# Performance work log

Hardware: AMD Instinct MI355X
Metric: run time of the kernel (lower is better)

Reference implementation:

```python
import jax, jax.numpy as jnp
import numpy as np

H, Hh, E, V, OUT, B, S, T, PAD = 512, 256, 512, 50000, 512, 64, 128, 128, 0


def setup_inputs() -> dict:
    key = jax.random.key(0)
    ks = iter(jax.random.split(key, 32))

    def p(shape, scale=0.05):
        return jax.random.normal(next(ks), shape, jnp.float32) * scale

    emb_in = p((V, E)).at[PAD].set(0.0)   # padding_idx row is zero
    emb_out = p((V, E)).at[PAD].set(0.0)
    src_tokens = jax.random.randint(next(ks), (B, S), 1, V)  # avoid pad_idx=0
    dst = jax.random.randint(next(ks), (B, T), 1, V)
    return {
        'src_tokens': src_tokens,
        'src_lengths': jnp.full((B,), S, dtype=jnp.int32),  # full lengths -> pack/pad is identity
        'dst': dst,
        'emb_in': emb_in, 'emb_out': emb_out,
        'enc_w_ih0': p((2, 4 * Hh, E)),   # [dir, 4h, in] layer0
        'enc_w_ih1': p((2, 4 * Hh, H)),   # layer1 input is bidir concat (H)
        'enc_w_hh': p((2, 2, 4 * Hh, Hh)),  # [layer, dir, 4h, h]
        'enc_b_ih': p((2, 2, 4 * Hh)),
        'enc_b_hh': p((2, 2, 4 * Hh)),
        'dec_w_ih0': p((4 * H, H + E)), 'dec_w_hh0': p((4 * H, H)),
        'dec_b_ih0': p((4 * H,)), 'dec_b_hh0': p((4 * H,)),
        'dec_w_ih1': p((4 * H, H)), 'dec_w_hh1': p((4 * H, H)),
        'dec_b_ih1': p((4 * H,)), 'dec_b_hh1': p((4 * H,)),
        'attn_w': p((H, 2 * H)),           # output_proj, bias=False
        'pred_w': p((OUT, H)), 'pred_b': p((OUT,)),
    }


def _lstm_cell(x, h, c, w_ih, w_hh, b_ih, b_hh):
    # torch gate order: i, f, g, o
    g = x @ w_ih.T + h @ w_hh.T + b_ih + b_hh
    i, f, gg, o = jnp.split(g, 4, axis=-1)
    c = jax.nn.sigmoid(f) * c + jax.nn.sigmoid(i) * jnp.tanh(gg)
    h = jax.nn.sigmoid(o) * jnp.tanh(c)
    return h, c


def _run_lstm(xs, w_ih, w_hh, b_ih, b_hh, reverse):
    z = jnp.zeros((xs.shape[1], w_hh.shape[1]), xs.dtype)

    def step(carry, x):
        h, c = _lstm_cell(x, carry[0], carry[1], w_ih, w_hh, b_ih, b_hh)
        return (h, c), h

    (h, c), out = jax.lax.scan(step, (z, z), xs, reverse=reverse)
    return out, h, c


def _forward(src_tokens, dst, emb_in, emb_out, enc_w_ih0, enc_w_ih1, enc_w_hh,
             enc_b_ih, enc_b_hh, dec_w_ih0, dec_w_hh0, dec_b_ih0, dec_b_hh0,
             dec_w_ih1, dec_w_hh1, dec_b_ih1, dec_b_hh1, attn_w, pred_w, pred_b):
    src = src_tokens.T          # [S, B]
    dst_t = dst.T               # [T, B]
    bsz = src.shape[1]

    # ---- Encoder: 2-layer bidirectional LSTM (sequences are full length) ----
    x = emb_in[src]             # [S, B, E]
    w_ihs = (enc_w_ih0, enc_w_ih1)
    fin_h, fin_c = [], []
    for l in range(2):
        outs = []
        for d, rev in ((0, False), (1, True)):
            o, h, c = _run_lstm(x, w_ihs[l][d], enc_w_hh[l, d], enc_b_ih[l, d], enc_b_hh[l, d], rev)
            outs.append(o)
            fin_h.append(h)
            fin_c.append(c)
        x = jnp.concatenate(outs, axis=-1)   # [S, B, H]
    enc_out = x
    # combine_bidir: per-layer concat of fwd/bwd final states -> [B, H]
    h_l0 = jnp.concatenate(fin_h[0:2], axis=-1)
    h_l1 = jnp.concatenate(fin_h[2:4], axis=-1)
    c_l0 = jnp.concatenate(fin_c[0:2], axis=-1)
    c_l1 = jnp.concatenate(fin_c[2:4], axis=-1)

    enc_mask = (src == PAD)     # [S, B]
    dst_emb = emb_out[dst_t]    # [T, B, E]

    # ---- Decoder: 2 stacked LSTMCells + dot-product attention, input feeding ----
    def dec_step(carry, emb_t):
        h0, c0, h1, c1, feed = carry
        inp = jnp.concatenate((emb_t, feed), axis=1)          # [B, E+H]
        h0, c0 = _lstm_cell(inp, h0, c0, dec_w_ih0, dec_w_hh0, dec_b_ih0, dec_b_hh0)
        h1, c1 = _lstm_cell(h0, h1, c1, dec_w_ih1, dec_w_hh1, dec_b_ih1, dec_b_hh1)
        scores = jnp.einsum('sbh,bh->sb', enc_out, h1)        # [S, B]
        scores = jnp.where(enc_mask, -jnp.inf, scores)
        attn = jax.nn.softmax(scores, axis=0)
        ctx = jnp.einsum('sb,sbh->bh', attn, enc_out)         # [B, H]
        out = jnp.tanh(jnp.concatenate((ctx, h1), axis=1) @ attn_w.T)
        return (h0, c0, h1, c1, out), out

    feed0 = jnp.zeros((bsz, H), dst_emb.dtype)
    _, outs = jax.lax.scan(dec_step, (h_l0, c_l0, h_l1, c_l1, feed0), dst_emb)  # [T, B, H]

    # pred_proj then transpose(1, 2) -> [B, OUT, T]
    res = jnp.einsum('tbh,oh->bot', outs, pred_w) + pred_b[None, :, None]
    return res


def reference(src_tokens, src_lengths, dst, emb_in, emb_out, enc_w_ih0, enc_w_ih1,
              enc_w_hh, enc_b_ih, enc_b_hh, dec_w_ih0, dec_w_hh0, dec_b_ih0,
              dec_b_hh0, dec_w_ih1, dec_w_hh1, dec_b_ih1, dec_b_hh1, attn_w,
              pred_w, pred_b):
    # src_lengths are all == S so pack_padded/pad_packed is an identity
    del src_lengths
    return _forward(src_tokens, dst, emb_in, emb_out, enc_w_ih0, enc_w_ih1,
                    enc_w_hh, enc_b_ih, enc_b_hh, dec_w_ih0, dec_w_hh0,
                    dec_b_ih0, dec_b_hh0, dec_w_ih1, dec_w_hh1, dec_b_ih1,
                    dec_b_hh1, attn_w, pred_w, pred_b)
```

## Files before the change

### kernel.cpp

```cpp
#include <hip/hip_runtime.h>
#include <hip/hip_bf16.h>

#define SS 128
#define TT 128
#define NBLK 256
#define NBD  128
#define FSTRIDE 16

typedef __attribute__((ext_vector_type(8))) short bf16x8;
typedef __attribute__((ext_vector_type(4))) float f32x4;
typedef unsigned short ushort_t;

__device__ __forceinline__ float sigf(float x) { return 1.f / (1.f + __expf(-x)); }

__device__ __forceinline__ ushort_t f2bf(float f) {
  unsigned b = __builtin_bit_cast(unsigned, f);
  return (ushort_t)((b + 0x7FFFu + ((b >> 16) & 1u)) >> 16);
}
__device__ __forceinline__ float bf2f(ushort_t u) {
  return __builtin_bit_cast(float, (unsigned)u << 16);
}

__device__ __forceinline__ void cstoreh(ushort_t* p, ushort_t v) {
  __hip_atomic_store(p, v, __ATOMIC_RELAXED, __HIP_MEMORY_SCOPE_AGENT);
}

__device__ __forceinline__ int xidx(int k, int b) {
  return (((k >> 5) * 256 + b * 4 + ((k >> 3) & 3)) << 3) + (k & 7);
}

template<int NB>
__device__ __forceinline__ void gbar(unsigned* flags, unsigned gen) {
  __syncthreads();
  int tid = threadIdx.x;
  if (tid == 0) {
    asm volatile("s_waitcnt vmcnt(0)" ::: "memory");
    __hip_atomic_store(&flags[blockIdx.x * FSTRIDE], gen, __ATOMIC_RELAXED,
                       __HIP_MEMORY_SCOPE_AGENT);
  }
  {
    int who = tid & (NB - 1);
    int guard = 0;
    while (__hip_atomic_load(&flags[who * FSTRIDE], __ATOMIC_RELAXED,
                             __HIP_MEMORY_SCOPE_AGENT) < gen &&
           ++guard < (1 << 20))
      __builtin_amdgcn_s_sleep(1);
  }
  __syncthreads();
  asm volatile("" ::: "memory");
}

__global__ void k_embed_bf(const float* __restrict__ emb, const int* __restrict__ toks,
                           ushort_t* __restrict__ out, int seqlen) {
  int s = blockIdx.x >> 6, b = blockIdx.x & 63;
  int tok = toks[b * seqlen + s];
  float4 v = ((const float4*)(emb + (size_t)tok * 512))[threadIdx.x];
  unsigned lo = (unsigned)f2bf(v.x) | ((unsigned)f2bf(v.y) << 16);
  unsigned hi = (unsigned)f2bf(v.z) | ((unsigned)f2bf(v.w) << 16);
  uint2 pk = {lo, hi};
  *(uint2*)&out[(size_t)blockIdx.x * 512 + threadIdx.x * 4] = pk;
}

__global__ void k_castw(const float* __restrict__ s0, const float* __restrict__ s1,
                        const float* __restrict__ s2, const float* __restrict__ s3,
                        ushort_t* __restrict__ wBF, ushort_t* __restrict__ predBF) {
  int row = blockIdx.x, which = blockIdx.y;
  if (which == 3 && row >= 512) return;
  const float* src = (which == 0) ? s0 + (size_t)row * 512
                   : (which == 1) ? s1 + (size_t)row * 512
                   : (which == 2) ? s2 + (size_t)row * 1024
                                  : s3 + (size_t)row * 512;
  float4 v = ((const float4*)src)[threadIdx.x];
  unsigned lo = (unsigned)f2bf(v.x) | ((unsigned)f2bf(v.y) << 16);
  unsigned hi = (unsigned)f2bf(v.z) | ((unsigned)f2bf(v.w) << 16);
  uint2 pk = {lo, hi};
  if (which == 3)
    *(uint2*)&predBF[(size_t)row * 512 + threadIdx.x * 4] = pk;
  else
    *(uint2*)&wBF[((size_t)which * 2048 + row) * 512 + threadIdx.x * 4] = pk;
}

__global__ __launch_bounds__(256) void gemm_bf(
    const ushort_t* __restrict__ X, const ushort_t* __restrict__ W,
    const float* __restrict__ b1, const float* __restrict__ b2,
    float* __restrict__ C, int MODE) {
  __shared__ ushort_t Xs[128 * 72];
  __shared__ ushort_t Ws[128 * 72];
  __shared__ float sbias[128];
  int n0 = blockIdx.x * 128, m0 = blockIdx.y * 128;
  int tid = threadIdx.x;
  int lane = tid & 63;
  int wv = __builtin_amdgcn_readfirstlane(tid >> 6);
  int h_m = (wv >> 1) * 64, h_n = (wv & 1) * 64;
  int l16 = lane & 15, l4 = (lane >> 4) * 4, k8 = (lane >> 4) * 8;
  if (tid < 128) sbias[tid] = b1[n0 + tid] + (b2 ? b2[n0 + tid] : 0.f);
  f32x4 acc[4][4] = {};
  int lrow = tid >> 1, lhf = (tid & 1) * 32;
  for (int k0 = 0; k0 < 512; k0 += 64) {
    __syncthreads();
    const ushort_t* xs = X + (size_t)(m0 + lrow) * 512 + k0 + lhf;
    const ushort_t* wsrc = W + (size_t)(n0 + lrow) * 512 + k0 + lhf;
#pragma unroll
    for (int q = 0; q < 4; ++q) {
      *(bf16x8*)&Xs[lrow * 72 + lhf + q * 8] = *(const bf16x8*)(xs + q * 8);
      *(bf16x8*)&Ws[lrow * 72 + lhf + q * 8] = *(const bf16x8*)(wsrc + q * 8);
    }
    __syncthreads();
#pragma unroll
    for (int kk = 0; kk < 2; ++kk) {
#pragma unroll
      for (int mt = 0; mt < 4; ++mt) {
        bf16x8 af = *(const bf16x8*)&Xs[(h_m + mt * 16 + l16) * 72 + kk * 32 + k8];
#pragma unroll
        for (int nt = 0; nt < 4; ++nt) {
          bf16x8 bf = *(const bf16x8*)&Ws[(h_n + nt * 16 + l16) * 72 + kk * 32 + k8];
          acc[mt][nt] = __builtin_amdgcn_mfma_f32_16x16x32_bf16(af, bf, acc[mt][nt], 0, 0, 0);
        }
      }
    }
  }
  if (MODE == 1) {
    int s = (m0 + h_m) >> 6;
#pragma unroll
    for (int nt = 0; nt < 4; ++nt) {
      int n = n0 + h_n + nt * 16 + l16;
      float bias = sbias[h_n + nt * 16 + l16];
#pragma unroll
      for (int mt = 0; mt < 4; ++mt) {
        f32x4 v = acc[mt][nt];
        v[0] += bias; v[1] += bias; v[2] += bias; v[3] += bias;
        *(f32x4*)&C[((size_t)s * 2048 + n) * 64 + mt * 16 + l4] = v;
      }
    }
  } else {
#pragma unroll
    for (int nt = 0; nt < 4; ++nt) {
      int n = n0 + h_n + nt * 16 + l16;
      float bias = sbias[h_n + nt * 16 + l16];
#pragma unroll
      for (int mt = 0; mt < 4; ++mt) {
#pragma unroll
        for (int r = 0; r < 4; ++r) {
          int m = m0 + h_m + mt * 16 + l4 + r;
          C[((size_t)(m & 63) * 512 + n) * 128 + (m >> 6)] = acc[mt][nt][r] + bias;
        }
      }
    }
  }
}

template<int LOUT>
__global__ __launch_bounds__(256, 1) void enc_persist(
    const float* __restrict__ GT,
    const float* __restrict__ whh,
    ushort_t* __restrict__ ringE,
    ushort_t* __restrict__ lout,
    ushort_t* __restrict__ hFin,
    float* __restrict__ cFin,
    unsigned* bar) {
  int nb = blockIdx.x;
  int d = nb >> 7, nbL = nb & 127;
  int tid = threadIdx.x;
  int lane = tid & 63;
  int wv = __builtin_amdgcn_readfirstlane(tid >> 6);
  int l16 = lane & 15, kg = lane >> 4;
  __shared__ ushort_t wE[16 * 264];

  for (int idx = tid; idx < 16 * 256; idx += 256) {
    int m = idx >> 8, k = idx & 255;
    float v = 0.f;
    if (m < 8)
      v = whh[(size_t)d * 262144 +
              (size_t)((m & 3) * 256 + nbL + 128 * (m >> 2)) * 256 + k];
    wE[m * 264 + k] = f2bf(v);
  }
  __syncthreads();

  int b = wv * 16 + l16;
  int hu = nbL + 128 * kg;
  float creg = 0.f;
  const ushort_t* wp = wE + l16 * 264 + kg * 8;

  for (int t = 0; t < SS; ++t) {
    int s = d ? (SS - 1 - t) : t;
    const ushort_t* xb = ringE + (size_t)(t * 2 + d) * 16384 +
                         wv * 512 + l16 * 32 + kg * 8;
    bf16x8 bfr[8];
#pragma unroll
    for (int ks = 0; ks < 8; ++ks) bfr[ks] = *(const bf16x8*)(xb + ks * 2048);
    float gi[4];
    if (lane < 32) {
#pragma unroll
      for (int r = 0; r < 4; ++r)
        gi[r] = GT[((size_t)s * 2048 + d * 1024 + r * 256 + hu) * 64 + b];
    }
    f32x4 acc = {0.f, 0.f, 0.f, 0.f};
#pragma unroll
    for (int ks = 0; ks < 8; ++ks) {
      bf16x8 af = *(const bf16x8*)(wp + ks * 32);
      acc = __builtin_amdgcn_mfma_f32_16x16x32_bf16(af, bfr[ks], acc, 0, 0, 0);
    }
    if (lane < 32) {
      float g4[4];
#pragma unroll
      for (int r = 0; r < 4; ++r) g4[r] = acc[r] + gi[r];
      float ig = sigf(g4[0]), fg = sigf(g4[1]), gg = tanhf(g4[2]), og = sigf(g4[3]);
      creg = fg * creg + ig * gg;
      float hn = og * tanhf(creg);
      cstoreh(&ringE[(size_t)((t + 1) * 2 + d) * 16384 + xidx(hu, b)], f2bf(hn));
      if (LOUT == 0)
        lout[((size_t)s * 64 + b) * 512 + d * 256 + hu] = f2bf(hn);
      else
        lout[(size_t)b * 65536 + (size_t)s * 512 + d * 256 + hu] = f2bf(hn);
      if (t == SS - 1) {
        hFin[xidx(512 + d * 256 + hu, b)] = f2bf(hn);
        cFin[(d * 256 + hu) * 64 + b] = creg;
      }
    }
    if (t < SS - 1) gbar<NBLK>(bar, (unsigned)(t + 1));
  }
}

__global__ __launch_bounds__(256, 1) void dec_persist(
    const float* __restrict__ GdT,
    const float* __restrict__ w_ih0, const float* __restrict__ w_hh0,
    const float* __restrict__ w_ih1, const float* __restrict__ w_hh1,
    const float* __restrict__ b_ih1, const float* __restrict__ b_hh1,
    const float* __restrict__ attn_w,
    const ushort_t* __restrict__ enc_out,
    const int* __restrict__ src_tokens,
    const float* __restrict__ c0T, const float* __restrict__ c1T,
    ushort_t* __restrict__ r0, ushort_t* __restrict__ r1,
    ushort_t* __restrict__ r2,
    ushort_t* __restrict__ houtsB,
    unsigned* bar) {
  int nb = blockIdx.x;
  int tid = threadIdx.x;
  int lane = tid & 63;
  int wv = __builtin_amdgcn_readfirstlane(tid >> 6);
  int l16 = lane & 15, kg = lane >> 4;
  __shared__ ushort_t wAl[16 * 1032];
  __shared__ ushort_t wBl[16 * 1032];
  __shared__ ushort_t wDl[16 * 1032];
  __shared__ float h1s[512];
  __shared__ float sc[128];

  for (int idx = tid; idx < 16384; idx += 256) {
    int m = idx >> 10, k = idx & 1023;
    int j = m >> 2, g = m & 3;
    int row = g * 512 + nb + 128 * j;
    float va = (k < 512) ? w_ih0[(size_t)row * 1024 + 512 + k]
                         : w_hh0[(size_t)row * 512 + (k - 512)];
    float vb = (k < 512) ? w_ih1[(size_t)row * 512 + k]
                         : w_hh1[(size_t)row * 512 + (k - 512)];
    float vd = (m < 4) ? attn_w[(size_t)(nb * 4 + m) * 1024 + k] : 0.f;
    wAl[m * 1032 + k] = f2bf(va);
    wBl[m * 1032 + k] = f2bf(vb);
    wDl[m * 1032 + k] = f2bf(vd);
  }
  __syncthreads();

  int b = wv * 16 + l16;
  int hu = nb + 128 * kg;
  float c0r = c0T[hu * 64 + b];
  float c1r = c1T[hu * 64 + b];
  float bias1[4];
#pragma unroll
  for (int r = 0; r < 4; ++r)
    bias1[r] = b_ih1[r * 512 + hu] + b_hh1[r * 512 + hu];
  const ushort_t* wpA = wAl + l16 * 1032 + kg * 8;
  const ushort_t* wpB = wBl + l16 * 1032 + kg * 8;
  const ushort_t* wpD = wDl + l16 * 1032 + kg * 8;
  int fragoff = wv * 512 + l16 * 32 + kg * 8;

  for (int t = 0; t < TT; ++t) {
    unsigned gb = (unsigned)(t * 4);
    size_t sC = (size_t)t * 65536, sN = (size_t)(t + 1) * 65536;
    {
      const ushort_t* xb = r0 + sC + fragoff;
      bf16x8 bfr[32];
#pragma unroll
      for (int ks = 0; ks < 32; ++ks) bfr[ks] = *(const bf16x8*)(xb + ks * 2048);
      float giA[4];
#pragma unroll
      for (int r = 0; r < 4; ++r)
        giA[r] = GdT[((size_t)t * 2048 + r * 512 + hu) * 64 + b];
      f32x4 acc = {0.f, 0.f, 0.f, 0.f};
#pragma unroll
      for (int ks = 0; ks < 32; ++ks) {
        bf16x8 af = *(const bf16x8*)(wpA + ks * 32);
        acc = __builtin_amdgcn_mfma_f32_16x16x32_bf16(af, bfr[ks], acc, 0, 0, 0);
      }
      float g4[4];
#pragma unroll
      for (int r = 0; r < 4; ++r) g4[r] = acc[r] + giA[r];
      float ig = sigf(g4[0]), fg = sigf(g4[1]), gg = tanhf(g4[2]), og = sigf(g4[3]);
      c0r = fg * c0r + ig * gg;
      float hn = og * tanhf(c0r);
      cstoreh(&r0[sN + xidx(512 + hu, b)], f2bf(hn));
    }
    gbar<NBD>(bar, gb + 1);
    {
      bf16x8 bfr[32];
      const ushort_t* xh0 = r0 + sN + fragoff;
      const ushort_t* xh1 = r1 + sC + fragoff;
#pragma unroll
      for (int ks = 0; ks < 16; ++ks) bfr[ks] = *(const bf16x8*)(xh0 + (16 + ks) * 2048);
#pragma unroll
      for (int ks = 16; ks < 32; ++ks) bfr[ks] = *(const bf16x8*)(xh1 + ks * 2048);
      f32x4 acc = {0.f, 0.f, 0.f, 0.f};
#pragma unroll
      for (int ks = 0; ks < 32; ++ks) {
        bf16x8 af = *(const bf16x8*)(wpB + ks * 32);
        acc = __builtin_amdgcn_mfma_f32_16x16x32_bf16(af, bfr[ks], acc, 0, 0, 0);
      }
      float g4[4];
#pragma unroll
      for (int r = 0; r < 4; ++r) g4[r] = acc[r] + bias1[r];
      float ig = sigf(g4[0]), fg = sigf(g4[1]), gg = tanhf(g4[2]), og = sigf(g4[3]);
      c1r = fg * c1r + ig * gg;
      float hn = og * tanhf(c1r);
      cstoreh(&r1[sN + xidx(512 + hu, b)], f2bf(hn));
    }
    gbar<NBD>(bar, gb + 2);
    if (nb < 64) {
      const ushort_t* eb = enc_out + (size_t)nb * 65536;
      for (int i = tid; i < 512; i += 256)
        h1s[i] = bf2f(r1[sN + xidx(512 + i, nb)]);
      __syncthreads();
      {
        int s2 = tid >> 1, half = tid & 1;
        const ushort_t* er = eb + (size_t)s2 * 512 + half * 256;
        const float* hh = h1s + half * 256;
        float a = 0.f;
#pragma unroll 4
        for (int k = 0; k < 256; k += 8) {
          bf16x8 ev = *(const bf16x8*)(er + k);
#pragma unroll
          for (int i = 0; i < 8; ++i)
            a += bf2f((ushort_t)ev[i]) * hh[k + i];
        }
        a += __shfl_xor(a, 1);
        if (!half) sc[s2] = (src_tokens[nb * SS + s2] == 0) ? -1e30f : a;
      }
      __syncthreads();
      if (tid < 64) {
        float m = fmaxf(sc[tid], sc[tid + 64]);
        for (int off = 32; off; off >>= 1) m = fmaxf(m, __shfl_xor(m, off));
        float e0 = __expf(sc[tid] - m), e1 = __expf(sc[tid + 64] - m);
        float ssum = e0 + e1;
        for (int off = 32; off; off >>= 1) ssum += __shfl_xor(ssum, off);
        float inv = 1.f / ssum;
        sc[tid] = e0 * inv; sc[tid + 64] = e1 * inv;
      }
      __syncthreads();
      float a0 = 0.f, a1 = 0.f;
      for (int s2 = 0; s2 < 128; ++s2) {
        float p_ = sc[s2];
        const ushort_t* er = eb + (size_t)s2 * 512;
        a0 += p_ * bf2f(er[tid]);
        a1 += p_ * bf2f(er[tid + 256]);
      }
      cstoreh(&r2[sC + xidx(tid, nb)], f2bf(a0));
      cstoreh(&r2[sC + xidx(tid + 256, nb)], f2bf(a1));
    }
    gbar<NBD>(bar, gb + 3);
    {
      bf16x8 bfr[32];
      const ushort_t* xc = r2 + sC + fragoff;
      const ushort_t* xh1 = r1 + sN + fragoff;
#pragma unroll
      for (int ks = 0; ks < 16; ++ks) bfr[ks] = *(const bf16x8*)(xc + ks * 2048);
#pragma unroll
      for (int ks = 16; ks < 32; ++ks) bfr[ks] = *(const bf16x8*)(xh1 + ks * 2048);
      f32x4 acc = {0.f, 0.f, 0.f, 0.f};
#pragma unroll
      for (int ks = 0; ks < 32; ++ks) {
        bf16x8 af = *(const bf16x8*)(wpD + ks * 32);
        acc = __builtin_amdgcn_mfma_f32_16x16x32_bf16(af, bfr[ks], acc, 0, 0, 0);
      }
      if (lane < 16) {
#pragma unroll
        for (int r = 0; r < 4; ++r) {
          int o = nb * 4 + r;
          float v = tanhf(acc[r]);
          ushort_t vb = f2bf(v);
          cstoreh(&r0[sN + xidx(o, b)], vb);
          houtsB[((size_t)t * 64 + b) * 512 + o] = vb;
        }
      }
    }
    if (t < TT - 1) gbar<NBD>(bar, gb + 4);
  }
}

extern "C" void kernel_launch(void* const* d_in, const int* in_sizes, int n_in,
                              void* d_out, int out_size, void* d_ws, size_t ws_size,
                              hipStream_t stream) {
  const int*   src_tokens = (const int*)d_in[0];
  const int*   dst        = (const int*)d_in[2];
  const float* emb_in     = (const float*)d_in[3];
  const float* emb_out    = (const float*)d_in[4];
  const float* enc_w_ih0  = (const float*)d_in[5];
  const float* enc_w_ih1  = (const float*)d_in[6];
  const float* enc_w_hh   = (const float*)d_in[7];
  const float* enc_b_ih   = (const float*)d_in[8];
  const float* enc_b_hh   = (const float*)d_in[9];
  const float* dec_w_ih0  = (const float*)d_in[10];
  const float* dec_w_hh0  = (const float*)d_in[11];
  const float* dec_b_ih0  = (const float*)d_in[12];
  const float* dec_b_hh0  = (const float*)d_in[13];
  const float* dec_w_ih1  = (const float*)d_in[14];
  const float* dec_w_hh1  = (const float*)d_in[15];
  const float* dec_b_ih1  = (const float*)d_in[16];
  const float* dec_b_hh1  = (const float*)d_in[17];
  const float* attn_w     = (const float*)d_in[18];
  const float* pred_w     = (const float*)d_in[19];
  const float* pred_b     = (const float*)d_in[20];
  float* out = (float*)d_out;

  float* ws       = (float*)d_ws;
  ushort_t* houtsB = (ushort_t*)ws;
  float* GT       = ws + 4194304;
  ushort_t* encOutB = (ushort_t*)(ws + 20971520);
  ushort_t* predBF  = (ushort_t*)(ws + 23068672);
  ushort_t* r0    = (ushort_t*)(ws + 25165824);
  ushort_t* r1    = (ushort_t*)(ws + 29392896);
  ushort_t* r2    = (ushort_t*)(ws + 33619968);
  ushort_t* wBF   = r2;
  ushort_t* ringE = (ushort_t*)(ws + 37814272);
  float* c0T      = ws + 39927808;
  float* c1T      = ws + 39960576;
  unsigned* barA  = (unsigned*)(ws + 39993344);
  unsigned* barB  = barA + 8192;
  unsigned* barC  = barB + 8192;
  ushort_t* U     = (ushort_t*)(ws + 40017920);

  hipMemsetAsync(barA, 0, 3 * 8192 * sizeof(unsigned), stream);
  hipMemsetAsync(r0, 0, 65536 * sizeof(ushort_t), stream);
  hipMemsetAsync(r1, 0, 65536 * sizeof(ushort_t), stream);
  hipMemsetAsync(ringE, 0, 32768 * sizeof(ushort_t), stream);

  k_castw<<<dim3(2048, 4), 128, 0, stream>>>(enc_w_ih0, enc_w_ih1, dec_w_ih0,
                                             pred_w, wBF, predBF);

  k_embed_bf<<<dim3(8192), 128, 0, stream>>>(emb_in, src_tokens, U, SS);
  gemm_bf<<<dim3(16, 64), 256, 0, stream>>>(U, wBF, enc_b_ih, enc_b_hh, GT, 1);
  enc_persist<0><<<dim3(NBLK), 256, 0, stream>>>(GT, enc_w_hh, ringE, U,
                                                 r0, c0T, barA);
  gemm_bf<<<dim3(16, 64), 256, 0, stream>>>(U, wBF + 1048576,
                                            enc_b_ih + 2048, enc_b_hh + 2048, GT, 1);
  enc_persist<1><<<dim3(NBLK), 256, 0, stream>>>(GT, enc_w_hh + 524288, ringE,
                                                 encOutB, r1, c1T, barB);

  k_embed_bf<<<dim3(8192), 128, 0, stream>>>(emb_out, dst, U, TT);
  gemm_bf<<<dim3(16, 64), 256, 0, stream>>>(U, wBF + 2097152,
                                            dec_b_ih0, dec_b_hh0, GT, 1);

  dec_persist<<<dim3(NBD), 256, 0, stream>>>(
      GT, dec_w_ih0, dec_w_hh0, dec_w_ih1, dec_w_hh1, dec_b_ih1, dec_b_hh1,
      attn_w, encOutB, src_tokens, c0T, c1T, r0, r1, r2, houtsB, barC);

  gemm_bf<<<dim3(4, 64), 256, 0, stream>>>(houtsB, predBF,
                                           pred_b, nullptr, out, 2);
}
```

Before: 4.367 ms.

## Compute attention output projection per batch row locally, removing one grid barrier per step

The decoder's attention output projection (tanh of [ctx,h1] times attn_w) no longer goes through a global ring buffer followed by a grid barrier and an MFMA matvec split across blocks. Each block now keeps its context vector in shared memory and computes all 512 outputs for its own batch row with scalar FMAs over a pre-transposed, packed bf16 copy of attn_w that k_castw builds. This removes one grid-wide barrier and a global round trip per timestep. In exchange each block reads the whole 1 MB weight from global/L2 every step and does the multiply-adds without MFMA.

```diff
diff --git a/kernel.cpp b/kernel.cpp
--- a/kernel.cpp
+++ b/kernel.cpp
@@ -63,9 +63,20 @@
 
 __global__ void k_castw(const float* __restrict__ s0, const float* __restrict__ s1,
                         const float* __restrict__ s2, const float* __restrict__ s3,
-                        ushort_t* __restrict__ wBF, ushort_t* __restrict__ predBF) {
+                        const float* __restrict__ s4,
+                        ushort_t* __restrict__ wBF, ushort_t* __restrict__ predBF,
+                        ushort_t* __restrict__ wTpk) {
   int row = blockIdx.x, which = blockIdx.y;
-  if (which == 3 && row >= 512) return;
+  if (which >= 3 && row >= 512) return;
+  if (which == 4) {
+    int o = row, k0 = threadIdx.x * 8;
+    ushort_t tmp[8];
+#pragma unroll
+    for (int i = 0; i < 8; ++i)
+      tmp[i] = f2bf(s4[(size_t)o * 1024 + k0 + i]);
+    *(bf16x8*)&wTpk[((size_t)threadIdx.x * 512 + o) * 8] = *(const bf16x8*)tmp;
+    return;
+  }
   const float* src = (which == 0) ? s0 + (size_t)row * 512
                    : (which == 1) ? s1 + (size_t)row * 512
                    : (which == 2) ? s2 + (size_t)row * 1024
@@ -226,12 +237,11 @@
     const float* __restrict__ w_ih0, const float* __restrict__ w_hh0,
     const float* __restrict__ w_ih1, const float* __restrict__ w_hh1,
     const float* __restrict__ b_ih1, const float* __restrict__ b_hh1,
-    const float* __restrict__ attn_w,
+    const ushort_t* __restrict__ wTpk,
     const ushort_t* __restrict__ enc_out,
     const int* __restrict__ src_tokens,
     const float* __restrict__ c0T, const float* __restrict__ c1T,
     ushort_t* __restrict__ r0, ushort_t* __restrict__ r1,
-    ushort_t* __restrict__ r2,
     ushort_t* __restrict__ houtsB,
     unsigned* bar) {
   int nb = blockIdx.x;
@@ -241,8 +251,8 @@
   int l16 = lane & 15, kg = lane >> 4;
   __shared__ ushort_t wAl[16 * 1032];
   __shared__ ushort_t wBl[16 * 1032];
-  __shared__ ushort_t wDl[16 * 1032];
   __shared__ float h1s[512];
+  __shared__ float ctxs[512];
   __shared__ float sc[128];
 
   for (int idx = tid; idx < 16384; idx += 256) {
@@ -253,10 +263,8 @@
                          : w_hh0[(size_t)row * 512 + (k - 512)];
     float vb = (k < 512) ? w_ih1[(size_t)row * 512 + k]
                          : w_hh1[(size_t)row * 512 + (k - 512)];
-    float vd = (m < 4) ? attn_w[(size_t)(nb * 4 + m) * 1024 + k] : 0.f;
     wAl[m * 1032 + k] = f2bf(va);
     wBl[m * 1032 + k] = f2bf(vb);
-    wDl[m * 1032 + k] = f2bf(vd);
   }
   __syncthreads();
 
@@ -270,11 +278,10 @@
     bias1[r] = b_ih1[r * 512 + hu] + b_hh1[r * 512 + hu];
   const ushort_t* wpA = wAl + l16 * 1032 + kg * 8;
   const ushort_t* wpB = wBl + l16 * 1032 + kg * 8;
-  const ushort_t* wpD = wDl + l16 * 1032 + kg * 8;
   int fragoff = wv * 512 + l16 * 32 + kg * 8;
 
   for (int t = 0; t < TT; ++t) {
-    unsigned gb = (unsigned)(t * 4);
+    unsigned gb = (unsigned)(t * 3);
     size_t sC = (size_t)t * 65536, sN = (size_t)(t + 1) * 65536;
     {
       const ushort_t* xb = r0 + sC + fragoff;
@@ -354,43 +361,42 @@
         sc[tid] = e0 * inv; sc[tid + 64] = e1 * inv;
       }
       __syncthreads();
-      float a0 = 0.f, a1 = 0.f;
-      for (int s2 = 0; s2 < 128; ++s2) {
-        float p_ = sc[s2];
-        const ushort_t* er = eb + (size_t)s2 * 512;
-        a0 += p_ * bf2f(er[tid]);
-        a1 += p_ * bf2f(er[tid + 256]);
-      }
-      cstoreh(&r2[sC + xidx(tid, nb)], f2bf(a0));
-      cstoreh(&r2[sC + xidx(tid + 256, nb)], f2bf(a1));
-    }
-    gbar<NBD>(bar, gb + 3);
-    {
-      bf16x8 bfr[32];
-      const ushort_t* xc = r2 + sC + fragoff;
-      const ushort_t* xh1 = r1 + sN + fragoff;
-#pragma unroll
-      for (int ks = 0; ks < 16; ++ks) bfr[ks] = *(const bf16x8*)(xc + ks * 2048);
-#pragma unroll
-      for (int ks = 16; ks < 32; ++ks) bfr[ks] = *(const bf16x8*)(xh1 + ks * 2048);
-      f32x4 acc = {0.f, 0.f, 0.f, 0.f};
-#pragma unroll
-      for (int ks = 0; ks < 32; ++ks) {
-        bf16x8 af = *(const bf16x8*)(wpD + ks * 32);
-        acc = __builtin_amdgcn_mfma_f32_16x16x32_bf16(af, bfr[ks], acc, 0, 0, 0);
-      }
-      if (lane < 16) {
-#pragma unroll
-        for (int r = 0; r < 4; ++r) {
-          int o = nb * 4 + r;
-          float v = tanhf(acc[r]);
-          ushort_t vb = f2bf(v);
-          cstoreh(&r0[sN + xidx(o, b)], vb);
-          houtsB[((size_t)t * 64 + b) * 512 + o] = vb;
+      {
+        float a0 = 0.f, a1 = 0.f;
+        for (int s2 = 0; s2 < 128; ++s2) {
+          float p_ = sc[s2];
+          const ushort_t* er = eb + (size_t)s2 * 512;
+          a0 += p_ * bf2f(er[tid]);
+          a1 += p_ * bf2f(er[tid + 256]);
         }
-      }
-    }
-    if (t < TT - 1) gbar<NBD>(bar, gb + 4);
+        ctxs[tid] = a0;
+        ctxs[tid + 256] = a1;
+      }
+      __syncthreads();
+      {
+        int o1 = tid, o2 = tid + 256;
+        float acc1 = 0.f, acc2 = 0.f;
+#pragma unroll 4
+        for (int c = 0; c < 128; ++c) {
+          const float* xk = (c < 64) ? &ctxs[c * 8] : &h1s[c * 8 - 512];
+          bf16x8 w1 = *(const bf16x8*)&wTpk[((size_t)c * 512 + o1) * 8];
+          bf16x8 w2 = *(const bf16x8*)&wTpk[((size_t)c * 512 + o2) * 8];
+#pragma unroll
+          for (int i = 0; i < 8; ++i) {
+            float xv = xk[i];
+            acc1 += bf2f((ushort_t)w1[i]) * xv;
+            acc2 += bf2f((ushort_t)w2[i]) * xv;
+          }
+        }
+        float v1 = tanhf(acc1), v2 = tanhf(acc2);
+        ushort_t vb1 = f2bf(v1), vb2 = f2bf(v2);
+        cstoreh(&r0[sN + xidx(o1, nb)], vb1);
+        cstoreh(&r0[sN + xidx(o2, nb)], vb2);
+        houtsB[((size_t)t * 64 + nb) * 512 + o1] = vb1;
+        houtsB[((size_t)t * 64 + nb) * 512 + o2] = vb2;
+      }
+    }
+    if (t < TT - 1) gbar<NBD>(bar, gb + 3);
   }
 }
 
@@ -424,6 +430,7 @@
   float* GT       = ws + 4194304;
   ushort_t* encOutB = (ushort_t*)(ws + 20971520);
   ushort_t* predBF  = (ushort_t*)(ws + 23068672);
+  ushort_t* wTpk    = (ushort_t*)(ws + 23199744);
   ushort_t* r0    = (ushort_t*)(ws + 25165824);
   ushort_t* r1    = (ushort_t*)(ws + 29392896);
   ushort_t* r2    = (ushort_t*)(ws + 33619968);
@@ -441,8 +448,8 @@
   hipMemsetAsync(r1, 0, 65536 * sizeof(ushort_t), stream);
   hipMemsetAsync(ringE, 0, 32768 * sizeof(ushort_t), stream);
 
-  k_castw<<<dim3(2048, 4), 128, 0, stream>>>(enc_w_ih0, enc_w_ih1, dec_w_ih0,
-                                             pred_w, wBF, predBF);
+  k_castw<<<dim3(2048, 5), 128, 0, stream>>>(enc_w_ih0, enc_w_ih1, dec_w_ih0,
+                                             pred_w, attn_w, wBF, predBF, wTpk);
 
   k_embed_bf<<<dim3(8192), 128, 0, stream>>>(emb_in, src_tokens, U, SS);
   gemm_bf<<<dim3(16, 64), 256, 0, stream>>>(U, wBF, enc_b_ih, enc_b_hh, GT, 1);
@@ -459,7 +466,7 @@
 
   dec_persist<<<dim3(NBD), 256, 0, stream>>>(
       GT, dec_w_ih0, dec_w_hh0, dec_w_ih1, dec_w_hh1, dec_b_ih1, dec_b_hh1,
-      attn_w, encOutB, src_tokens, c0T, c1T, r0, r1, r2, houtsB, barC);
+      wTpk, encOutB, src_tokens, c0T, c1T, r0, r1, houtsB, barC);
 
   gemm_bf<<<dim3(4, 64), 256, 0, stream>>>(houtsB, predBF,
                                            pred_b, nullptr, out, 2);
```

After: 5.053 ms. +15.7%, slower.
